# Kernel tuning notes

Hardware: AMD Instinct MI355X
Metric: run time of the kernel (lower is better)

The kernel has to match this reference:

```python
import jax, jax.numpy as jnp
import numpy as np

N = 1024
V = 3889   # SMAL mesh vertices
NJ = 33    # kinematic-tree joints
NR = 35    # rotations in theta (35*3 = 105)
NB = 41    # shape betas
PARENTS = np.concatenate([[0], np.arange(NJ - 1)]).astype(np.int32)  # parent[i] < i
EXTRA_VERT_IDS = np.array([1863, 26, 2124, 150, 3055, 1097])


def _beta_scale_mask():
    m = np.zeros((NR, 3, 6), np.float32)
    leg = list(range(7, 15)) + list(range(17, 25))
    tail = list(range(25, 32))
    ears = [33, 34]
    m[leg, 2, 0] = 1.0; m[leg, 0, 1] = 1.0; m[leg, 1, 1] = 1.0
    m[tail, 0, 2] = 1.0; m[tail, 1, 3] = 1.0; m[tail, 2, 3] = 1.0
    m[ears, 1, 4] = 1.0; m[ears, 2, 5] = 1.0
    return jnp.asarray(m.reshape(NR * 3, 6).T)  # (6, 105)

BETA_SCALE_MASK = _beta_scale_mask()


def batch_rodrigues(theta):
    # theta: (M, 3) axis-angle -> (M, 3, 3) rotation matrices
    angle = jnp.linalg.norm(theta + 1e-8, axis=1, keepdims=True)  # (M,1)
    r = theta / angle
    c = jnp.cos(angle)[..., None]
    s = jnp.sin(angle)[..., None]
    outer = r[:, :, None] * r[:, None, :]
    z = jnp.zeros_like(r[:, 0])
    rx, ry, rz = r[:, 0], r[:, 1], r[:, 2]
    H = jnp.stack([z, -rz, ry, rz, z, -rx, -ry, rx, z], axis=1).reshape(-1, 3, 3)
    eye = jnp.eye(3, dtype=theta.dtype)
    return c * eye + (1.0 - c) * outer + s * H


def make_A(R, t):
    # R: (n,3,3), t: (n,3) -> homogeneous (n,4,4)
    top = jnp.concatenate([R, t[..., None]], axis=-1)
    bottom = jnp.broadcast_to(jnp.array([0.0, 0.0, 0.0, 1.0], dtype=R.dtype), (R.shape[0], 1, 4))
    return jnp.concatenate([top, bottom], axis=1)


def smal_forward(beta, theta, trans, betas_logscale, shapedirs, v_template, J_regressor, posedirs, weights):
    n = beta.shape[0]
    v_shaped = v_template + (beta @ shapedirs).reshape(n, V, 3)           # (n,V,3)
    J = jnp.einsum('nva,vj->nja', v_shaped, J_regressor)                  # (n,33,3)
    Rs = batch_rodrigues(theta.reshape(-1, 3)).reshape(n, NR, 3, 3)
    # pose blendshape term: original multiplies an all-zero pose_feature by posedirs
    v_posed = v_shaped + (jnp.zeros((1, 288), v_shaped.dtype) @ posedirs).reshape(1, V, 3)
    # per-joint anisotropic log-scales
    scal = jnp.exp(betas_logscale @ BETA_SCALE_MASK).reshape(n, NR, 3)    # (n,35,3)
    # kinematic chain (fixed 33-joint loop with parent dependency)
    results = [make_A(Rs[:, 0], J[:, 0])]
    for i in range(1, NJ):
        p = int(PARENTS[i])
        j_here = J[:, i] - J[:, p]
        # diag(1/s_parent) @ R @ diag(s_i), exact inverse of diagonal scale
        rot_new = Rs[:, i] * scal[:, i][:, None, :] / scal[:, p][:, :, None]
        results.append(results[p] @ make_A(rot_new, j_here))
    results = jnp.stack(results, axis=1)                                   # (n,33,4,4)
    init_bone = jnp.einsum('njxk,njk->njx', results[..., :3], J)           # (n,33,4)
    A = jnp.concatenate([results[..., :3], (results[..., 3] - init_bone)[..., None]], axis=-1)
    # linear blend skinning
    T = jnp.einsum('vj,njk->nvk', weights, A.reshape(n, NJ, 16)).reshape(n, V, 4, 4)
    v_homo = jnp.concatenate([v_posed * jnp.ones((n, 1, 1), v_posed.dtype),
                              jnp.ones((n, V, 1), v_posed.dtype)], axis=-1)
    verts = jnp.einsum('nvab,nvb->nva', T, v_homo)[..., :3] + trans[:, None, :]
    joints = jnp.einsum('nva,vj->nja', verts, J_regressor)                 # (n,33,3)
    joints = jnp.concatenate([joints, verts[:, EXTRA_VERT_IDS]], axis=1)   # (n,39,3)
    return verts, joints


def setup_inputs() -> dict:
    key = jax.random.key(0)
    ks = jax.random.split(key, 9)
    return {
        'beta': jax.random.normal(ks[0], (N, NB), jnp.float32) * 0.1,
        'theta': jax.random.normal(ks[1], (N, NR * 3), jnp.float32) * 0.2,
        'trans': jax.random.normal(ks[2], (N, 3), jnp.float32),
        'betas_logscale': jax.random.normal(ks[3], (N, 6), jnp.float32) * 0.1,
        'shapedirs': jax.random.normal(ks[4], (NB, V * 3), jnp.float32) * 0.01,
        'v_template': jax.random.normal(ks[5], (V, 3), jnp.float32),
        'J_regressor': jax.random.uniform(ks[6], (V, NJ), jnp.float32) / V,
        'posedirs': jax.random.normal(ks[7], (288, V * 3), jnp.float32) * 0.01,
        'weights': jax.random.uniform(ks[8], (V, NJ), jnp.float32),
    }


def reference(beta, theta, trans, betas_logscale, shapedirs, v_template, J_regressor, posedirs, weights):
    return smal_forward(beta, theta, trans, betas_logscale, shapedirs, v_template, J_regressor, posedirs, weights)
```

## Files before the change

### kernel.cpp

```cpp
#include <hip/hip_runtime.h>
#include <hip/hip_bf16.h>

#define NV 3889
#define NV3 11667
#define NVP 3904
#define NVAP 11712
#define NJC 33
#define NBB 41
#define NN 1024

__device__ const int EXTRA_IDS[6] = {1863, 26, 2124, 150, 3055, 1097};

#define WS_SJ    0
#define WS_WPK   4160
#define WS_SDPK  129088
#define WS_BPK   503872
#define WS_APK   536640
#define WS_JTL   929856
#define WS_VTL   1028160
#define WS_SJP   13611072

typedef __attribute__((ext_vector_type(8))) short short8v;
typedef __attribute__((ext_vector_type(4))) float f32x4;

__device__ __forceinline__ ushort bf16bits(float x) {
  __hip_bfloat16 h = __float2bfloat16(x);
  return *reinterpret_cast<ushort*>(&h);
}

#define PREP_PACK_BLOCKS 9536
__global__ void __launch_bounds__(256) k_prep(
    const float* __restrict__ Jreg, const float* __restrict__ w,
    const float* __restrict__ beta, const float* __restrict__ sd,
    const float* __restrict__ vt, float* __restrict__ ws) {
  if (blockIdx.x < PREP_PACK_BLOCKS) {
    int id = blockIdx.x * 256 + threadIdx.x;
    const int S1 = NVP * 64;
    const int S2 = NVAP * 64;
    const int S3 = NN * 64;
    const int S4 = 3 * 128 * 512;
    const int S5 = 192 * 6144;
    if (id < S1) {
      int v = id >> 6, j = id & 63;
      float val;
      if (j < NJC)      val = (v < NV) ? w[v * NJC + j] : 0.f;
      else if (j == 41) val = 1.f;
      else              val = 0.f;
      ((__hip_bfloat16*)(ws + WS_WPK))[id] = __float2bfloat16(val);
      return;
    }
    id -= S1;
    if (id < S2) {
      int va = id >> 6, bs = id & 63;
      float val = 0.f;
      if (va < NV3) {
        if (bs < NBB)       val = sd[(size_t)bs * NV3 + va];
        else if (bs == NBB) val = vt[va];
      }
      ((__hip_bfloat16*)(ws + WS_SDPK))[id] = __float2bfloat16(val);
      return;
    }
    id -= S2;
    if (id < S3) {
      int n = id >> 6, bs = id & 63;
      float val = (bs < NBB) ? beta[n * NBB + bs] : (bs == NBB ? 1.f : 0.f);
      ((__hip_bfloat16*)(ws + WS_BPK))[id] = __float2bfloat16(val);
      return;
    }
    id -= S3;
    if (id < S4) {
      int tile = id >> 9, sub = id & 511;
      int lane = sub >> 3, e = sub & 7;
      int jt = tile >> 7, kc = tile & 127;
      int j = jt * 16 + (lane & 15);
      int v = kc * 32 + ((lane >> 4) << 3) + e;
      float val = (j < NJC && v < NV) ? Jreg[v * NJC + j] : 0.f;
      ((__hip_bfloat16*)(ws + WS_JTL))[id] = __float2bfloat16(val);
      return;
    }
    id -= S4;
    if (id < S5) {
      int plane = id / 6144, rem = id - plane * 6144;
      ((ushort*)(ws + WS_VTL))[(size_t)plane * 131072 + 122 * 1024 + rem] = 0;
    }
    return;
  }
  int bid2 = blockIdx.x - PREP_PACK_BLOCKS;
  int b = bid2 >> 4, c = bid2 & 15;
  const float* src = (b < NBB) ? (sd + (size_t)b * NV3) : vt;
  int t = threadIdx.x;
  int dv = t / 33, j = t - dv * 33;
  float p0 = 0.f, p1 = 0.f, p2 = 0.f;
  int vbase = c * 244;
  int vend = vbase + 244;
  if (vend > NV) vend = NV;
  if (t < 231) {
    for (int v0 = vbase; v0 < vend; v0 += 7) {
      int v = v0 + dv;
      if (v < vend) {
        float jr = Jreg[v0 * 33 + t];
        p0 += src[v * 3 + 0] * jr;
        p1 += src[v * 3 + 1] * jr;
        p2 += src[v * 3 + 2] * jr;
      }
    }
  }
  __shared__ float sred[7][33][3];
  if (t < 231) { sred[dv][j][0] = p0; sred[dv][j][1] = p1; sred[dv][j][2] = p2; }
  __syncthreads();
  if (t < 99) {
    int jj = t / 3, aa = t - jj * 3;
    float s = 0.f;
#pragma unroll
    for (int d = 0; d < 7; d++) s += sred[d][jj][aa];
    ws[WS_SJP + bid2 * 100 + t] = s;
  }
}

__global__ void __launch_bounds__(256) k_sjr(float* __restrict__ ws) {
  int idx = blockIdx.x * 256 + threadIdx.x;
  if (idx >= 42 * 99) return;
  int b = idx / 99, k = idx - b * 99;
  float s = 0.f;
#pragma unroll
  for (int c = 0; c < 16; c++) s += ws[WS_SJP + (b * 16 + c) * 100 + k];
  ws[WS_SJ + idx] = s;
}

__device__ __forceinline__ void get_scal(int r, float e0, float e1, float e2, float e3,
                                         float s[3]) {
  bool leg  = (r >= 7 && r <= 14) || (r >= 17 && r <= 24);
  bool tail = (r >= 25 && r <= 31);
  s[0] = leg ? e1 : (tail ? e2 : 1.f);
  s[1] = leg ? e1 : (tail ? e3 : 1.f);
  s[2] = leg ? e0 : (tail ? e3 : 1.f);
}

__device__ __forceinline__ void rodrigues(const float* th, float R[9]) {
  float tx = th[0], ty = th[1], tz = th[2];
  float ax = tx + 1e-8f, ay = ty + 1e-8f, az = tz + 1e-8f;
  float angle = sqrtf(ax * ax + ay * ay + az * az);
  float inv = 1.f / angle;
  float rx = tx * inv, ry = ty * inv, rz = tz * inv;
  float c = cosf(angle), s = sinf(angle), o = 1.f - c;
  R[0] = c + o * rx * rx;      R[1] = o * rx * ry - s * rz; R[2] = o * rx * rz + s * ry;
  R[3] = o * rx * ry + s * rz; R[4] = c + o * ry * ry;      R[5] = o * ry * rz - s * rx;
  R[6] = o * rx * rz - s * ry; R[7] = o * ry * rz + s * rx; R[8] = c + o * rz * rz;
}

__global__ void __launch_bounds__(128) k_pose(
    const float* __restrict__ beta, const float* __restrict__ theta,
    const float* __restrict__ bls, const float* __restrict__ trans,
    float* __restrict__ ws) {
  int n = blockIdx.x, t = threadIdx.x;
  __shared__ float Jsh[99];
  __shared__ float Bsh[NJC * 12];
  __shared__ float Ash[NJC * 12];
  if (t < 99) {
    const float* SJ = ws + WS_SJ;
    float acc = SJ[NBB * 99 + t];
    const float* bn = beta + n * NBB;
#pragma unroll
    for (int b = 0; b < NBB; b++) acc += bn[b] * SJ[b * 99 + t];
    Jsh[t] = acc;
  }
  __syncthreads();
  if (t < NJC) {
    float R[9];
    rodrigues(theta + n * 105 + t * 3, R);
    float* B = Bsh + t * 12;
    if (t == 0) {
      B[0] = R[0]; B[1] = R[1]; B[2]  = R[2]; B[3]  = Jsh[0];
      B[4] = R[3]; B[5] = R[4]; B[6]  = R[5]; B[7]  = Jsh[1];
      B[8] = R[6]; B[9] = R[7]; B[10] = R[8]; B[11] = Jsh[2];
    } else {
      float e0 = expf(bls[n * 6 + 0]), e1 = expf(bls[n * 6 + 1]);
      float e2 = expf(bls[n * 6 + 2]), e3 = expf(bls[n * 6 + 3]);
      float si[3], sp[3];
      get_scal(t, e0, e1, e2, e3, si);
      get_scal(t - 1, e0, e1, e2, e3, sp);
#pragma unroll
      for (int r = 0; r < 3; r++) {
        float inv = 1.f / sp[r];
#pragma unroll
        for (int cc = 0; cc < 3; cc++) B[r * 4 + cc] = R[r * 3 + cc] * si[cc] * inv;
        B[r * 4 + 3] = Jsh[t * 3 + r] - Jsh[(t - 1) * 3 + r];
      }
    }
  }
  __syncthreads();
  if (t == 0) {
    float G[12];
#pragma unroll
    for (int k = 0; k < 12; k++) G[k] = Bsh[k];
#pragma unroll
    for (int i = 0; i < NJC; i++) {
      if (i > 0) {
        float b[12];
#pragma unroll
        for (int k = 0; k < 12; k++) b[k] = Bsh[i * 12 + k];
        float Gn[12];
#pragma unroll
        for (int r = 0; r < 3; r++) {
#pragma unroll
          for (int cc = 0; cc < 4; cc++) {
            float acc = G[r * 4 + 0] * b[0 * 4 + cc] + G[r * 4 + 1] * b[1 * 4 + cc] +
                        G[r * 4 + 2] * b[2 * 4 + cc];
            if (cc == 3) acc += G[r * 4 + 3];
            Gn[r * 4 + cc] = acc;
          }
        }
#pragma unroll
        for (int k = 0; k < 12; k++) G[k] = Gn[k];
      }
      float jx = Jsh[i * 3 + 0], jy = Jsh[i * 3 + 1], jz = Jsh[i * 3 + 2];
      float* Ai = Ash + i * 12;
      Ai[0] = G[0]; Ai[1] = G[1]; Ai[2]  = G[2];
      Ai[3] = G[3] - (G[0] * jx + G[1] * jy + G[2] * jz);
      Ai[4] = G[4]; Ai[5] = G[5]; Ai[6]  = G[6];
      Ai[7] = G[7] - (G[4] * jx + G[5] * jy + G[6] * jz);
      Ai[8] = G[8]; Ai[9] = G[9]; Ai[10] = G[10];
      Ai[11] = G[11] - (G[8] * jx + G[9] * jy + G[10] * jz);
    }
  }
  __syncthreads();
  __hip_bfloat16* apk = (__hip_bfloat16*)(ws + WS_APK) + (size_t)n * 768;
  for (int i = t; i < 768; i += 128) {
    int c = i >> 6, j = i & 63;
    float val = 0.f;
    if (j < NJC)                           val = Ash[j * 12 + c];
    else if (j == 41 && (c & 3) == 3)      val = trans[n * 3 + (c >> 2)];
    apk[i] = __float2bfloat16(val);
  }
}

#define ASH_USH (16 * 12 * 72)
#define VSL2_USH (2 * 16 * 72)

__global__ void __launch_bounds__(512, 4) k_sv(
    const float* __restrict__ ws, ushort* __restrict__ vst,
    float* __restrict__ out) {
  __shared__ __align__(16) ushort lds[ASH_USH + 8 * VSL2_USH];
  int wv = threadIdx.x >> 6, lane = threadIdx.x & 63;
  int g = lane >> 4, c16 = lane & 15;
  int p = blockIdx.x * 8 + wv;
  int pc = p < 122 ? p : 121;
  bool pok = p < 122;
  int vtA = pc * 2, vtB = vtA + 1;
  int vA = vtA * 16 + c16, vB = vtB * 16 + c16;
  int nb0 = blockIdx.y * 32;
  const ushort* Wp = (const ushort*)(ws + WS_WPK);
  const ushort* Sp = (const ushort*)(ws + WS_SDPK);
  const ushort* Bp = (const ushort*)(ws + WS_BPK);
  const ushort* Ap = (const ushort*)(ws + WS_APK);

  short8v wfA0 = *(const short8v*)(Wp + vA * 64 + g * 8);
  short8v wfA1 = *(const short8v*)(Wp + vA * 64 + 32 + g * 8);
  short8v wfB0 = *(const short8v*)(Wp + vB * 64 + g * 8);
  short8v wfB1 = *(const short8v*)(Wp + vB * 64 + 32 + g * 8);
  int vaA = vtA * 48 + c16, vaB = vtB * 48 + c16;

  ushort* vslA = lds + ASH_USH + wv * VSL2_USH;
  ushort* vslB = vslA + 1152;
  bool act = g < 3;
  int hiA = c16 >> 3, hiB = 2 + (c16 >> 3), e8 = c16 & 7;

#pragma unroll 1
  for (int ch = 0; ch < 2; ch++) {
    int nb = nb0 + ch * 16;
    {
      const uint4* srcq = (const uint4*)(Ap + (size_t)nb * 768);
      for (int e = threadIdx.x; e < 1536; e += 512) {
        int r = e >> 3, col = e & 7;
        uint4 x = srcq[e];
        *(uint4*)(lds + r * 72 + col * 8) = x;
      }
    }
    short8v bf0 = *(const short8v*)(Bp + (size_t)(nb + c16) * 64 + g * 8);
    short8v bf1 = *(const short8v*)(Bp + (size_t)(nb + c16) * 64 + 32 + g * 8);
    short8v sfA00 = *(const short8v*)(Sp + (size_t)(vaA +  0) * 64 + g * 8);
    short8v sfA01 = *(const short8v*)(Sp + (size_t)(vaA +  0) * 64 + 32 + g * 8);
    short8v sfA10 = *(const short8v*)(Sp + (size_t)(vaA + 16) * 64 + g * 8);
    short8v sfA11 = *(const short8v*)(Sp + (size_t)(vaA + 16) * 64 + 32 + g * 8);
    short8v sfA20 = *(const short8v*)(Sp + (size_t)(vaA + 32) * 64 + g * 8);
    short8v sfA21 = *(const short8v*)(Sp + (size_t)(vaA + 32) * 64 + 32 + g * 8);
    short8v sfB00 = *(const short8v*)(Sp + (size_t)(vaB +  0) * 64 + g * 8);
    short8v sfB01 = *(const short8v*)(Sp + (size_t)(vaB +  0) * 64 + 32 + g * 8);
    short8v sfB10 = *(const short8v*)(Sp + (size_t)(vaB + 16) * 64 + g * 8);
    short8v sfB11 = *(const short8v*)(Sp + (size_t)(vaB + 16) * 64 + 32 + g * 8);
    short8v sfB20 = *(const short8v*)(Sp + (size_t)(vaB + 32) * 64 + g * 8);
    short8v sfB21 = *(const short8v*)(Sp + (size_t)(vaB + 32) * 64 + 32 + g * 8);
    f32x4 aA0 = {0,0,0,0}, aA1 = {0,0,0,0}, aA2 = {0,0,0,0};
    f32x4 aB0 = {0,0,0,0}, aB1 = {0,0,0,0}, aB2 = {0,0,0,0};
    aA0 = __builtin_amdgcn_mfma_f32_16x16x32_bf16(sfA00, bf0, aA0, 0, 0, 0);
    aA0 = __builtin_amdgcn_mfma_f32_16x16x32_bf16(sfA01, bf1, aA0, 0, 0, 0);
    aA1 = __builtin_amdgcn_mfma_f32_16x16x32_bf16(sfA10, bf0, aA1, 0, 0, 0);
    aA1 = __builtin_amdgcn_mfma_f32_16x16x32_bf16(sfA11, bf1, aA1, 0, 0, 0);
    aA2 = __builtin_amdgcn_mfma_f32_16x16x32_bf16(sfA20, bf0, aA2, 0, 0, 0);
    aA2 = __builtin_amdgcn_mfma_f32_16x16x32_bf16(sfA21, bf1, aA2, 0, 0, 0);
    aB0 = __builtin_amdgcn_mfma_f32_16x16x32_bf16(sfB00, bf0, aB0, 0, 0, 0);
    aB0 = __builtin_amdgcn_mfma_f32_16x16x32_bf16(sfB01, bf1, aB0, 0, 0, 0);
    aB1 = __builtin_amdgcn_mfma_f32_16x16x32_bf16(sfB10, bf0, aB1, 0, 0, 0);
    aB1 = __builtin_amdgcn_mfma_f32_16x16x32_bf16(sfB11, bf1, aB1, 0, 0, 0);
    aB2 = __builtin_amdgcn_mfma_f32_16x16x32_bf16(sfB20, bf0, aB2, 0, 0, 0);
    aB2 = __builtin_amdgcn_mfma_f32_16x16x32_bf16(sfB21, bf1, aB2, 0, 0, 0);
    {
      int wb = c16 * 72;
#pragma unroll
      for (int r = 0; r < 4; r++) {
        int rho = g * 4 + r;
        vslA[wb + (rho / 3) * 4 + (rho % 3)] = bf16bits(aA0[r]);
        vslB[wb + (rho / 3) * 4 + (rho % 3)] = bf16bits(aB0[r]);
      }
#pragma unroll
      for (int r = 0; r < 4; r++) {
        int rho = 16 + g * 4 + r;
        vslA[wb + (rho / 3) * 4 + (rho % 3)] = bf16bits(aA1[r]);
        vslB[wb + (rho / 3) * 4 + (rho % 3)] = bf16bits(aB1[r]);
      }
#pragma unroll
      for (int r = 0; r < 4; r++) {
        int rho = 32 + g * 4 + r;
        vslA[wb + (rho / 3) * 4 + (rho % 3)] = bf16bits(aA2[r]);
        vslB[wb + (rho / 3) * 4 + (rho % 3)] = bf16bits(aB2[r]);
      }
    }
    __syncthreads();

    int nt_w = nb >> 4;
    size_t tbg = ((size_t)((act ? g : 0) * 64 + nt_w) * 128 + pc) * 1024;
#pragma unroll 4
    for (int np = 0; np < 16; np++) {
      const ushort* an = lds + np * 864 + c16 * 72 + g * 8;
      short8v af0 = *(const short8v*)(an);
      short8v af1 = *(const short8v*)(an + 32);
      f32x4 accA = {0,0,0,0}, accB = {0,0,0,0};
      accA = __builtin_amdgcn_mfma_f32_16x16x32_bf16(af0, wfA0, accA, 0, 0, 0);
      accA = __builtin_amdgcn_mfma_f32_16x16x32_bf16(af1, wfA1, accA, 0, 0, 0);
      accB = __builtin_amdgcn_mfma_f32_16x16x32_bf16(af0, wfB0, accB, 0, 0, 0);
      accB = __builtin_amdgcn_mfma_f32_16x16x32_bf16(af1, wfB1, accB, 0, 0, 0);
      uint2 qA = *(const uint2*)(vslA + np * 72 + c16 * 4);
      uint2 qB = *(const uint2*)(vslB + np * 72 + c16 * 4);
      float sxA = __uint_as_float((qA.x & 0xffffu) << 16);
      float syA = __uint_as_float(qA.x & 0xffff0000u);
      float szA = __uint_as_float((qA.y & 0xffffu) << 16);
      float sxB = __uint_as_float((qB.x & 0xffffu) << 16);
      float syB = __uint_as_float(qB.x & 0xffff0000u);
      float szB = __uint_as_float((qB.y & 0xffffu) << 16);
      float rA = fmaf(accA[0], sxA, fmaf(accA[1], syA, fmaf(accA[2], szA, accA[3])));
      float rB = fmaf(accB[0], sxB, fmaf(accB[1], syB, fmaf(accB[2], szB, accB[3])));
      if (pok && act) {
        vst[tbg + (size_t)((hiA * 16 + np) * 8 + e8)] = bf16bits(rA);
        vst[tbg + (size_t)((hiB * 16 + np) * 8 + e8)] = bf16bits(rB);
        out[((size_t)(nb + np) * NV + vA) * 3 + g] = rA;
        if (vB < NV) out[((size_t)(nb + np) * NV + vB) * 3 + g] = rB;
      }
    }
    __syncthreads();
  }
}

__global__ void __launch_bounds__(256) k_jg2(
    const float* __restrict__ ws, const float* __restrict__ verts,
    float* __restrict__ jout) {
  __shared__ float red[4][48][16];
  int nt = blockIdx.x, a = blockIdx.y;
  int wv = threadIdx.x >> 6, lane = threadIdx.x & 63;
  const ushort* Jt = (const ushort*)(ws + WS_JTL);
  const ushort* Vt = (const ushort*)(ws + WS_VTL) + ((size_t)(a * 64 + nt) << 17);
  f32x4 acc0 = {0,0,0,0};
  f32x4 acc1 = {0,0,0,0};
  f32x4 acc2 = {0,0,0,0};
#pragma unroll 4
  for (int i = 0; i < 32; i++) {
    int kc = wv * 32 + i;
    short8v bfr = *(const short8v*)(Vt + ((size_t)kc << 10) + lane * 8);
    short8v af0 = *(const short8v*)(Jt + ((size_t)(0 * 128 + kc) << 9) + lane * 8);
    short8v af1 = *(const short8v*)(Jt + ((size_t)(1 * 128 + kc) << 9) + lane * 8);
    short8v af2 = *(const short8v*)(Jt + ((size_t)(2 * 128 + kc) << 9) + lane * 8);
    acc0 = __builtin_amdgcn_mfma_f32_16x16x32_bf16(af0, bfr, acc0, 0, 0, 0);
    acc1 = __builtin_amdgcn_mfma_f32_16x16x32_bf16(af1, bfr, acc1, 0, 0, 0);
    acc2 = __builtin_amdgcn_mfma_f32_16x16x32_bf16(af2, bfr, acc2, 0, 0, 0);
  }
  int hi = lane >> 4, c16 = lane & 15;
#pragma unroll
  for (int r = 0; r < 4; r++) {
    red[wv][ 0 + hi * 4 + r][c16] = acc0[r];
    red[wv][16 + hi * 4 + r][c16] = acc1[r];
    red[wv][32 + hi * 4 + r][c16] = acc2[r];
  }
  __syncthreads();
  for (int idx = threadIdx.x; idx < NJC * 16; idx += 256) {
    int j = idx >> 4, np = idx & 15;
    float s = red[0][j][np] + red[1][j][np] + red[2][j][np] + red[3][j][np];
    jout[(nt * 16 + np) * 117 + j * 3 + a] = s;
  }
  if (threadIdx.x < 96) {
    int e = threadIdx.x >> 4, np = threadIdx.x & 15;
    int n = nt * 16 + np;
    jout[n * 117 + 99 + e * 3 + a] = verts[(size_t)n * NV3 + EXTRA_IDS[e] * 3 + a];
  }
}

extern "C" void kernel_launch(void* const* d_in, const int* in_sizes, int n_in,
                              void* d_out, int out_size, void* d_ws, size_t ws_size,
                              hipStream_t stream) {
  const float* beta       = (const float*)d_in[0];
  const float* theta      = (const float*)d_in[1];
  const float* trans      = (const float*)d_in[2];
  const float* bls        = (const float*)d_in[3];
  const float* shapedirs  = (const float*)d_in[4];
  const float* v_template = (const float*)d_in[5];
  const float* Jreg       = (const float*)d_in[6];
  const float* weights    = (const float*)d_in[8];
  float* out = (float*)d_out;
  float* ws  = (float*)d_ws;
  float* jout = out + (size_t)NN * NV3;

  k_prep<<<PREP_PACK_BLOCKS + 672, 256, 0, stream>>>(Jreg, weights, beta,
                                                     shapedirs, v_template, ws);
  k_sjr<<<17, 256, 0, stream>>>(ws);
  k_pose<<<NN, 128, 0, stream>>>(beta, theta, bls, trans, ws);
  dim3 gsv(16, 32);
  k_sv<<<gsv, 512, 0, stream>>>(ws, (ushort*)(ws + WS_VTL), out);
  dim3 gj(64, 3);
  k_jg2<<<gj, 256, 0, stream>>>(ws, out, jout);
}
```

Before: 75.91 us.

## Fuse joint regression into skinning kernel and drop bf16 vertex staging buffer

```diff
diff --git a/kernel.cpp b/kernel.cpp
--- a/kernel.cpp
+++ b/kernel.cpp
@@ -17,8 +17,7 @@
 #define WS_BPK   503872
 #define WS_APK   536640
 #define WS_JTL   929856
-#define WS_VTL   1028160
-#define WS_SJP   13611072
+#define WS_JPART 1028160
 
 typedef __attribute__((ext_vector_type(8))) short short8v;
 typedef __attribute__((ext_vector_type(4))) float f32x4;
@@ -28,76 +27,88 @@
   return *reinterpret_cast<ushort*>(&h);
 }
 
-#define PREP_PACK_BLOCKS 9536
+#define PREP_PACK_BLOCKS 616
 __global__ void __launch_bounds__(256) k_prep(
     const float* __restrict__ Jreg, const float* __restrict__ w,
     const float* __restrict__ beta, const float* __restrict__ sd,
     const float* __restrict__ vt, float* __restrict__ ws) {
   if (blockIdx.x < PREP_PACK_BLOCKS) {
-    int id = blockIdx.x * 256 + threadIdx.x;
-    const int S1 = NVP * 64;
-    const int S2 = NVAP * 64;
-    const int S3 = NN * 64;
-    const int S4 = 3 * 128 * 512;
-    const int S5 = 192 * 6144;
-    if (id < S1) {
-      int v = id >> 6, j = id & 63;
-      float val;
-      if (j < NJC)      val = (v < NV) ? w[v * NJC + j] : 0.f;
-      else if (j == 41) val = 1.f;
-      else              val = 0.f;
-      ((__hip_bfloat16*)(ws + WS_WPK))[id] = __float2bfloat16(val);
+    int id8 = blockIdx.x * 256 + threadIdx.x;
+    const int R1 = NVP * 64 / 8;
+    const int R2 = NVAP * 64 / 8;
+    const int R3 = NN * 64 / 8;
+    short8v pk;
+    if (id8 < R1) {
+      int u = id8 * 8;
+      int v = u >> 6, j0 = u & 63;
+#pragma unroll
+      for (int e = 0; e < 8; e++) {
+        int j = j0 + e;
+        float val;
+        if (j < NJC)      val = (v < NV) ? w[v * NJC + j] : 0.f;
+        else if (j == 41) val = 1.f;
+        else              val = 0.f;
+        pk[e] = (short)bf16bits(val);
+      }
+      *(short8v*)((ushort*)(ws + WS_WPK) + u) = pk;
       return;
     }
-    id -= S1;
-    if (id < S2) {
-      int va = id >> 6, bs = id & 63;
-      float val = 0.f;
-      if (va < NV3) {
-        if (bs < NBB)       val = sd[(size_t)bs * NV3 + va];
-        else if (bs == NBB) val = vt[va];
-      }
-      ((__hip_bfloat16*)(ws + WS_SDPK))[id] = __float2bfloat16(val);
+    id8 -= R1;
+    if (id8 < R2) {
+      int u = id8 * 8;
+      int va = u >> 6, bs0 = u & 63;
+#pragma unroll
+      for (int e = 0; e < 8; e++) {
+        int bs = bs0 + e;
+        float val = 0.f;
+        if (va < NV3) {
+          if (bs < NBB)       val = sd[(size_t)bs * NV3 + va];
+          else if (bs == NBB) val = vt[va];
+        }
+        pk[e] = (short)bf16bits(val);
+      }
+      *(short8v*)((ushort*)(ws + WS_SDPK) + u) = pk;
       return;
     }
-    id -= S2;
-    if (id < S3) {
-      int n = id >> 6, bs = id & 63;
-      float val = (bs < NBB) ? beta[n * NBB + bs] : (bs == NBB ? 1.f : 0.f);
-      ((__hip_bfloat16*)(ws + WS_BPK))[id] = __float2bfloat16(val);
+    id8 -= R2;
+    if (id8 < R3) {
+      int u = id8 * 8;
+      int n = u >> 6, bs0 = u & 63;
+#pragma unroll
+      for (int e = 0; e < 8; e++) {
+        int bs = bs0 + e;
+        float val = (bs < NBB) ? beta[n * NBB + bs] : (bs == NBB ? 1.f : 0.f);
+        pk[e] = (short)bf16bits(val);
+      }
+      *(short8v*)((ushort*)(ws + WS_BPK) + u) = pk;
       return;
     }
-    id -= S3;
-    if (id < S4) {
-      int tile = id >> 9, sub = id & 511;
-      int lane = sub >> 3, e = sub & 7;
+    id8 -= R3;
+    {
+      int u = id8 * 8;
+      int tile = u >> 9, lane = (u >> 3) & 63;
       int jt = tile >> 7, kc = tile & 127;
       int j = jt * 16 + (lane & 15);
-      int v = kc * 32 + ((lane >> 4) << 3) + e;
-      float val = (j < NJC && v < NV) ? Jreg[v * NJC + j] : 0.f;
-      ((__hip_bfloat16*)(ws + WS_JTL))[id] = __float2bfloat16(val);
+      int vb = kc * 32 + ((lane >> 4) << 3);
+#pragma unroll
+      for (int e = 0; e < 8; e++) {
+        int v = vb + e;
+        float val = (j < NJC && v < NV) ? Jreg[v * NJC + j] : 0.f;
+        pk[e] = (short)bf16bits(val);
+      }
+      *(short8v*)((ushort*)(ws + WS_JTL) + u) = pk;
       return;
     }
-    id -= S4;
-    if (id < S5) {
-      int plane = id / 6144, rem = id - plane * 6144;
-      ((ushort*)(ws + WS_VTL))[(size_t)plane * 131072 + 122 * 1024 + rem] = 0;
-    }
-    return;
-  }
-  int bid2 = blockIdx.x - PREP_PACK_BLOCKS;
-  int b = bid2 >> 4, c = bid2 & 15;
+  }
+  int b = blockIdx.x - PREP_PACK_BLOCKS;
   const float* src = (b < NBB) ? (sd + (size_t)b * NV3) : vt;
   int t = threadIdx.x;
   int dv = t / 33, j = t - dv * 33;
   float p0 = 0.f, p1 = 0.f, p2 = 0.f;
-  int vbase = c * 244;
-  int vend = vbase + 244;
-  if (vend > NV) vend = NV;
   if (t < 231) {
-    for (int v0 = vbase; v0 < vend; v0 += 7) {
+    for (int v0 = 0; v0 < NV; v0 += 7) {
       int v = v0 + dv;
-      if (v < vend) {
+      if (v < NV) {
         float jr = Jreg[v0 * 33 + t];
         p0 += src[v * 3 + 0] * jr;
         p1 += src[v * 3 + 1] * jr;
@@ -113,18 +124,8 @@
     float s = 0.f;
 #pragma unroll
     for (int d = 0; d < 7; d++) s += sred[d][jj][aa];
-    ws[WS_SJP + bid2 * 100 + t] = s;
-  }
-}
-
-__global__ void __launch_bounds__(256) k_sjr(float* __restrict__ ws) {
-  int idx = blockIdx.x * 256 + threadIdx.x;
-  if (idx >= 42 * 99) return;
-  int b = idx / 99, k = idx - b * 99;
-  float s = 0.f;
-#pragma unroll
-  for (int c = 0; c < 16; c++) s += ws[WS_SJP + (b * 16 + c) * 100 + k];
-  ws[WS_SJ + idx] = s;
+    ws[WS_SJ + b * 99 + t] = s;
+  }
 }
 
 __device__ __forceinline__ void get_scal(int r, float e0, float e1, float e2, float e3,
@@ -235,171 +236,191 @@
 }
 
 #define ASH_USH (16 * 12 * 72)
-#define VSL2_USH (2 * 16 * 72)
-
-__global__ void __launch_bounds__(512, 4) k_sv(
-    const float* __restrict__ ws, ushort* __restrict__ vst,
-    float* __restrict__ out) {
-  __shared__ __align__(16) ushort lds[ASH_USH + 8 * VSL2_USH];
+#define VSL_USH (2 * 16 * 72)
+
+__global__ void __launch_bounds__(512, 4) k_sv2(
+    const float* __restrict__ ws, float* __restrict__ jpart,
+    float* __restrict__ out, float* __restrict__ jout) {
+  __shared__ __align__(16) ushort lds[ASH_USH + 8 * VSL_USH];
   int wv = threadIdx.x >> 6, lane = threadIdx.x & 63;
   int g = lane >> 4, c16 = lane & 15;
-  int p = blockIdx.x * 8 + wv;
-  int pc = p < 122 ? p : 121;
-  bool pok = p < 122;
-  int vtA = pc * 2, vtB = vtA + 1;
-  int vA = vtA * 16 + c16, vB = vtB * 16 + c16;
-  int nb0 = blockIdx.y * 32;
+  int pg = blockIdx.x;
+  int nc = blockIdx.y;
+  int nb = nc * 16;
   const ushort* Wp = (const ushort*)(ws + WS_WPK);
   const ushort* Sp = (const ushort*)(ws + WS_SDPK);
   const ushort* Bp = (const ushort*)(ws + WS_BPK);
   const ushort* Ap = (const ushort*)(ws + WS_APK);
-
-  short8v wfA0 = *(const short8v*)(Wp + vA * 64 + g * 8);
-  short8v wfA1 = *(const short8v*)(Wp + vA * 64 + 32 + g * 8);
-  short8v wfB0 = *(const short8v*)(Wp + vB * 64 + g * 8);
-  short8v wfB1 = *(const short8v*)(Wp + vB * 64 + 32 + g * 8);
-  int vaA = vtA * 48 + c16, vaB = vtB * 48 + c16;
-
-  ushort* vslA = lds + ASH_USH + wv * VSL2_USH;
+  const ushort* Jt = (const ushort*)(ws + WS_JTL);
+
+  {
+    const uint4* srcq = (const uint4*)(Ap + (size_t)nb * 768);
+    for (int e = threadIdx.x; e < 1536; e += 512) {
+      uint4 x = srcq[e];
+      *(uint4*)(lds + (e >> 3) * 72 + (e & 7) * 8) = x;
+    }
+  }
+  __syncthreads();
+
+  short8v bf0 = *(const short8v*)(Bp + (size_t)(nb + c16) * 64 + g * 8);
+  short8v bf1 = *(const short8v*)(Bp + (size_t)(nb + c16) * 64 + 32 + g * 8);
+
+  ushort* vslA = lds + ASH_USH + wv * VSL_USH;
   ushort* vslB = vslA + 1152;
   bool act = g < 3;
-  int hiA = c16 >> 3, hiB = 2 + (c16 >> 3), e8 = c16 & 7;
+
+  f32x4 jc00 = {0,0,0,0}, jc10 = {0,0,0,0}, jc20 = {0,0,0,0};
+  f32x4 jc01 = {0,0,0,0}, jc11 = {0,0,0,0}, jc21 = {0,0,0,0};
+  f32x4 jc02 = {0,0,0,0}, jc12 = {0,0,0,0}, jc22 = {0,0,0,0};
 
 #pragma unroll 1
-  for (int ch = 0; ch < 2; ch++) {
-    int nb = nb0 + ch * 16;
-    {
-      const uint4* srcq = (const uint4*)(Ap + (size_t)nb * 768);
-      for (int e = threadIdx.x; e < 1536; e += 512) {
-        int r = e >> 3, col = e & 7;
-        uint4 x = srcq[e];
-        *(uint4*)(lds + r * 72 + col * 8) = x;
-      }
-    }
-    short8v bf0 = *(const short8v*)(Bp + (size_t)(nb + c16) * 64 + g * 8);
-    short8v bf1 = *(const short8v*)(Bp + (size_t)(nb + c16) * 64 + 32 + g * 8);
-    short8v sfA00 = *(const short8v*)(Sp + (size_t)(vaA +  0) * 64 + g * 8);
-    short8v sfA01 = *(const short8v*)(Sp + (size_t)(vaA +  0) * 64 + 32 + g * 8);
-    short8v sfA10 = *(const short8v*)(Sp + (size_t)(vaA + 16) * 64 + g * 8);
-    short8v sfA11 = *(const short8v*)(Sp + (size_t)(vaA + 16) * 64 + 32 + g * 8);
-    short8v sfA20 = *(const short8v*)(Sp + (size_t)(vaA + 32) * 64 + g * 8);
-    short8v sfA21 = *(const short8v*)(Sp + (size_t)(vaA + 32) * 64 + 32 + g * 8);
-    short8v sfB00 = *(const short8v*)(Sp + (size_t)(vaB +  0) * 64 + g * 8);
-    short8v sfB01 = *(const short8v*)(Sp + (size_t)(vaB +  0) * 64 + 32 + g * 8);
-    short8v sfB10 = *(const short8v*)(Sp + (size_t)(vaB + 16) * 64 + g * 8);
-    short8v sfB11 = *(const short8v*)(Sp + (size_t)(vaB + 16) * 64 + 32 + g * 8);
-    short8v sfB20 = *(const short8v*)(Sp + (size_t)(vaB + 32) * 64 + g * 8);
-    short8v sfB21 = *(const short8v*)(Sp + (size_t)(vaB + 32) * 64 + 32 + g * 8);
-    f32x4 aA0 = {0,0,0,0}, aA1 = {0,0,0,0}, aA2 = {0,0,0,0};
-    f32x4 aB0 = {0,0,0,0}, aB1 = {0,0,0,0}, aB2 = {0,0,0,0};
-    aA0 = __builtin_amdgcn_mfma_f32_16x16x32_bf16(sfA00, bf0, aA0, 0, 0, 0);
-    aA0 = __builtin_amdgcn_mfma_f32_16x16x32_bf16(sfA01, bf1, aA0, 0, 0, 0);
-    aA1 = __builtin_amdgcn_mfma_f32_16x16x32_bf16(sfA10, bf0, aA1, 0, 0, 0);
-    aA1 = __builtin_amdgcn_mfma_f32_16x16x32_bf16(sfA11, bf1, aA1, 0, 0, 0);
-    aA2 = __builtin_amdgcn_mfma_f32_16x16x32_bf16(sfA20, bf0, aA2, 0, 0, 0);
-    aA2 = __builtin_amdgcn_mfma_f32_16x16x32_bf16(sfA21, bf1, aA2, 0, 0, 0);
-    aB0 = __builtin_amdgcn_mfma_f32_16x16x32_bf16(sfB00, bf0, aB0, 0, 0, 0);
-    aB0 = __builtin_amdgcn_mfma_f32_16x16x32_bf16(sfB01, bf1, aB0, 0, 0, 0);
-    aB1 = __builtin_amdgcn_mfma_f32_16x16x32_bf16(sfB10, bf0, aB1, 0, 0, 0);
-    aB1 = __builtin_amdgcn_mfma_f32_16x16x32_bf16(sfB11, bf1, aB1, 0, 0, 0);
-    aB2 = __builtin_amdgcn_mfma_f32_16x16x32_bf16(sfB20, bf0, aB2, 0, 0, 0);
-    aB2 = __builtin_amdgcn_mfma_f32_16x16x32_bf16(sfB21, bf1, aB2, 0, 0, 0);
-    {
-      int wb = c16 * 72;
-#pragma unroll
-      for (int r = 0; r < 4; r++) {
-        int rho = g * 4 + r;
-        vslA[wb + (rho / 3) * 4 + (rho % 3)] = bf16bits(aA0[r]);
-        vslB[wb + (rho / 3) * 4 + (rho % 3)] = bf16bits(aB0[r]);
-      }
-#pragma unroll
-      for (int r = 0; r < 4; r++) {
-        int rho = 16 + g * 4 + r;
-        vslA[wb + (rho / 3) * 4 + (rho % 3)] = bf16bits(aA1[r]);
-        vslB[wb + (rho / 3) * 4 + (rho % 3)] = bf16bits(aB1[r]);
-      }
-#pragma unroll
-      for (int r = 0; r < 4; r++) {
-        int rho = 32 + g * 4 + r;
-        vslA[wb + (rho / 3) * 4 + (rho % 3)] = bf16bits(aA2[r]);
-        vslB[wb + (rho / 3) * 4 + (rho % 3)] = bf16bits(aB2[r]);
-      }
-    }
-    __syncthreads();
-
-    int nt_w = nb >> 4;
-    size_t tbg = ((size_t)((act ? g : 0) * 64 + nt_w) * 128 + pc) * 1024;
+  for (int r = 0; r < 2; r++) {
+    int p = pg * 16 + r * 8 + wv;
+    if (p < 122) {
+      int vtA = p * 2, vtB = vtA + 1;
+      int vA = vtA * 16 + c16, vB = vtB * 16 + c16;
+      int vaA = vtA * 48 + c16, vaB = vtB * 48 + c16;
+      {
+        short8v s00 = *(const short8v*)(Sp + (size_t)(vaA +  0) * 64 + g * 8);
+        short8v s01 = *(const short8v*)(Sp + (size_t)(vaA +  0) * 64 + 32 + g * 8);
+        short8v s10 = *(const short8v*)(Sp + (size_t)(vaA + 16) * 64 + g * 8);
+        short8v s11 = *(const short8v*)(Sp + (size_t)(vaA + 16) * 64 + 32 + g * 8);
+        short8v s20 = *(const short8v*)(Sp + (size_t)(vaA + 32) * 64 + g * 8);
+        short8v s21 = *(const short8v*)(Sp + (size_t)(vaA + 32) * 64 + 32 + g * 8);
+        f32x4 a0 = {0,0,0,0}, a1 = {0,0,0,0}, a2 = {0,0,0,0};
+        a0 = __builtin_amdgcn_mfma_f32_16x16x32_bf16(s00, bf0, a0, 0, 0, 0);
+        a0 = __builtin_amdgcn_mfma_f32_16x16x32_bf16(s01, bf1, a0, 0, 0, 0);
+        a1 = __builtin_amdgcn_mfma_f32_16x16x32_bf16(s10, bf0, a1, 0, 0, 0);
+        a1 = __builtin_amdgcn_mfma_f32_16x16x32_bf16(s11, bf1, a1, 0, 0, 0);
+        a2 = __builtin_amdgcn_mfma_f32_16x16x32_bf16(s20, bf0, a2, 0, 0, 0);
+        a2 = __builtin_amdgcn_mfma_f32_16x16x32_bf16(s21, bf1, a2, 0, 0, 0);
+        int wb = c16 * 72;
+#pragma unroll
+        for (int rr = 0; rr < 4; rr++) {
+          int rho = g * 4 + rr;
+          vslA[wb + (rho / 3) * 4 + (rho % 3)] = bf16bits(a0[rr]);
+          rho = 16 + g * 4 + rr;
+          vslA[wb + (rho / 3) * 4 + (rho % 3)] = bf16bits(a1[rr]);
+          rho = 32 + g * 4 + rr;
+          vslA[wb + (rho / 3) * 4 + (rho % 3)] = bf16bits(a2[rr]);
+        }
+      }
+      {
+        short8v s00 = *(const short8v*)(Sp + (size_t)(vaB +  0) * 64 + g * 8);
+        short8v s01 = *(const short8v*)(Sp + (size_t)(vaB +  0) * 64 + 32 + g * 8);
+        short8v s10 = *(const short8v*)(Sp + (size_t)(vaB + 16) * 64 + g * 8);
+        short8v s11 = *(const short8v*)(Sp + (size_t)(vaB + 16) * 64 + 32 + g * 8);
+        short8v s20 = *(const short8v*)(Sp + (size_t)(vaB + 32) * 64 + g * 8);
+        short8v s21 = *(const short8v*)(Sp + (size_t)(vaB + 32) * 64 + 32 + g * 8);
+        f32x4 a0 = {0,0,0,0}, a1 = {0,0,0,0}, a2 = {0,0,0,0};
+        a0 = __builtin_amdgcn_mfma_f32_16x16x32_bf16(s00, bf0, a0, 0, 0, 0);
+        a0 = __builtin_amdgcn_mfma_f32_16x16x32_bf16(s01, bf1, a0, 0, 0, 0);
+        a1 = __builtin_amdgcn_mfma_f32_16x16x32_bf16(s10, bf0, a1, 0, 0, 0);
+        a1 = __builtin_amdgcn_mfma_f32_16x16x32_bf16(s11, bf1, a1, 0, 0, 0);
+        a2 = __builtin_amdgcn_mfma_f32_16x16x32_bf16(s20, bf0, a2, 0, 0, 0);
+        a2 = __builtin_amdgcn_mfma_f32_16x16x32_bf16(s21, bf1, a2, 0, 0, 0);
+        int wb = c16 * 72;
+#pragma unroll
+        for (int rr = 0; rr < 4; rr++) {
+          int rho = g * 4 + rr;
+          vslB[wb + (rho / 3) * 4 + (rho % 3)] = bf16bits(a0[rr]);
+          rho = 16 + g * 4 + rr;
+          vslB[wb + (rho / 3) * 4 + (rho % 3)] = bf16bits(a1[rr]);
+          rho = 32 + g * 4 + rr;
+          vslB[wb + (rho / 3) * 4 + (rho % 3)] = bf16bits(a2[rr]);
+        }
+      }
+      short8v wfA0 = *(const short8v*)(Wp + (size_t)vA * 64 + g * 8);
+      short8v wfA1 = *(const short8v*)(Wp + (size_t)vA * 64 + 32 + g * 8);
+      short8v wfB0 = *(const short8v*)(Wp + (size_t)vB * 64 + g * 8);
+      short8v wfB1 = *(const short8v*)(Wp + (size_t)vB * 64 + 32 + g * 8);
+      int exA = -1, exB = -1;
+#pragma unroll
+      for (int e = 0; e < 6; e++) {
+        if (vA == EXTRA_IDS[e]) exA = e;
+        if (vB == EXTRA_IDS[e]) exB = e;
+      }
 #pragma unroll 4
-    for (int np = 0; np < 16; np++) {
-      const ushort* an = lds + np * 864 + c16 * 72 + g * 8;
-      short8v af0 = *(const short8v*)(an);
-      short8v af1 = *(const short8v*)(an + 32);
-      f32x4 accA = {0,0,0,0}, accB = {0,0,0,0};
-      accA = __builtin_amdgcn_mfma_f32_16x16x32_bf16(af0, wfA0, accA, 0, 0, 0);
-      accA = __builtin_amdgcn_mfma_f32_16x16x32_bf16(af1, wfA1, accA, 0, 0, 0);
-      accB = __builtin_amdgcn_mfma_f32_16x16x32_bf16(af0, wfB0, accB, 0, 0, 0);
-      accB = __builtin_amdgcn_mfma_f32_16x16x32_bf16(af1, wfB1, accB, 0, 0, 0);
-      uint2 qA = *(const uint2*)(vslA + np * 72 + c16 * 4);
-      uint2 qB = *(const uint2*)(vslB + np * 72 + c16 * 4);
-      float sxA = __uint_as_float((qA.x & 0xffffu) << 16);
-      float syA = __uint_as_float(qA.x & 0xffff0000u);
-      float szA = __uint_as_float((qA.y & 0xffffu) << 16);
-      float sxB = __uint_as_float((qB.x & 0xffffu) << 16);
-      float syB = __uint_as_float(qB.x & 0xffff0000u);
-      float szB = __uint_as_float((qB.y & 0xffffu) << 16);
-      float rA = fmaf(accA[0], sxA, fmaf(accA[1], syA, fmaf(accA[2], szA, accA[3])));
-      float rB = fmaf(accB[0], sxB, fmaf(accB[1], syB, fmaf(accB[2], szB, accB[3])));
-      if (pok && act) {
-        vst[tbg + (size_t)((hiA * 16 + np) * 8 + e8)] = bf16bits(rA);
-        vst[tbg + (size_t)((hiB * 16 + np) * 8 + e8)] = bf16bits(rB);
-        out[((size_t)(nb + np) * NV + vA) * 3 + g] = rA;
-        if (vB < NV) out[((size_t)(nb + np) * NV + vB) * 3 + g] = rB;
-      }
-    }
-    __syncthreads();
-  }
-}
-
-__global__ void __launch_bounds__(256) k_jg2(
-    const float* __restrict__ ws, const float* __restrict__ verts,
-    float* __restrict__ jout) {
-  __shared__ float red[4][48][16];
-  int nt = blockIdx.x, a = blockIdx.y;
-  int wv = threadIdx.x >> 6, lane = threadIdx.x & 63;
-  const ushort* Jt = (const ushort*)(ws + WS_JTL);
-  const ushort* Vt = (const ushort*)(ws + WS_VTL) + ((size_t)(a * 64 + nt) << 17);
-  f32x4 acc0 = {0,0,0,0};
-  f32x4 acc1 = {0,0,0,0};
-  f32x4 acc2 = {0,0,0,0};
-#pragma unroll 4
-  for (int i = 0; i < 32; i++) {
-    int kc = wv * 32 + i;
-    short8v bfr = *(const short8v*)(Vt + ((size_t)kc << 10) + lane * 8);
-    short8v af0 = *(const short8v*)(Jt + ((size_t)(0 * 128 + kc) << 9) + lane * 8);
-    short8v af1 = *(const short8v*)(Jt + ((size_t)(1 * 128 + kc) << 9) + lane * 8);
-    short8v af2 = *(const short8v*)(Jt + ((size_t)(2 * 128 + kc) << 9) + lane * 8);
-    acc0 = __builtin_amdgcn_mfma_f32_16x16x32_bf16(af0, bfr, acc0, 0, 0, 0);
-    acc1 = __builtin_amdgcn_mfma_f32_16x16x32_bf16(af1, bfr, acc1, 0, 0, 0);
-    acc2 = __builtin_amdgcn_mfma_f32_16x16x32_bf16(af2, bfr, acc2, 0, 0, 0);
-  }
-  int hi = lane >> 4, c16 = lane & 15;
-#pragma unroll
-  for (int r = 0; r < 4; r++) {
-    red[wv][ 0 + hi * 4 + r][c16] = acc0[r];
-    red[wv][16 + hi * 4 + r][c16] = acc1[r];
-    red[wv][32 + hi * 4 + r][c16] = acc2[r];
-  }
-  __syncthreads();
-  for (int idx = threadIdx.x; idx < NJC * 16; idx += 256) {
-    int j = idx >> 4, np = idx & 15;
-    float s = red[0][j][np] + red[1][j][np] + red[2][j][np] + red[3][j][np];
-    jout[(nt * 16 + np) * 117 + j * 3 + a] = s;
-  }
-  if (threadIdx.x < 96) {
-    int e = threadIdx.x >> 4, np = threadIdx.x & 15;
-    int n = nt * 16 + np;
-    jout[n * 117 + 99 + e * 3 + a] = verts[(size_t)n * NV3 + EXTRA_IDS[e] * 3 + a];
-  }
+      for (int np = 0; np < 16; np++) {
+        const ushort* an = lds + np * 864 + c16 * 72 + g * 8;
+        short8v af0 = *(const short8v*)(an);
+        short8v af1 = *(const short8v*)(an + 32);
+        f32x4 accA = {0,0,0,0}, accB = {0,0,0,0};
+        accA = __builtin_amdgcn_mfma_f32_16x16x32_bf16(af0, wfA0, accA, 0, 0, 0);
+        accA = __builtin_amdgcn_mfma_f32_16x16x32_bf16(af1, wfA1, accA, 0, 0, 0);
+        accB = __builtin_amdgcn_mfma_f32_16x16x32_bf16(af0, wfB0, accB, 0, 0, 0);
+        accB = __builtin_amdgcn_mfma_f32_16x16x32_bf16(af1, wfB1, accB, 0, 0, 0);
+        uint2 qA = *(const uint2*)(vslA + np * 72 + c16 * 4);
+        uint2 qB = *(const uint2*)(vslB + np * 72 + c16 * 4);
+        float sxA = __uint_as_float((qA.x & 0xffffu) << 16);
+        float syA = __uint_as_float(qA.x & 0xffff0000u);
+        float szA = __uint_as_float((qA.y & 0xffffu) << 16);
+        float sxB = __uint_as_float((qB.x & 0xffffu) << 16);
+        float syB = __uint_as_float(qB.x & 0xffff0000u);
+        float szB = __uint_as_float((qB.y & 0xffffu) << 16);
+        float rA = fmaf(accA[0], sxA, fmaf(accA[1], syA, fmaf(accA[2], szA, accA[3])));
+        float rB = fmaf(accB[0], sxB, fmaf(accB[1], syB, fmaf(accB[2], szB, accB[3])));
+        if (act) {
+          out[((size_t)(nb + np) * NV + vA) * 3 + g] = rA;
+          if (vB < NV) out[((size_t)(nb + np) * NV + vB) * 3 + g] = rB;
+          if (exA >= 0) jout[(size_t)(nb + np) * 117 + 99 + exA * 3 + g] = rA;
+          if (exB >= 0) jout[(size_t)(nb + np) * 117 + 99 + exB * 3 + g] = rB;
+          ushort* dst = (g < 2) ? (vslA + np * 72 + g * 32) : (vslB + np * 72);
+          dst[c16]      = bf16bits(rA);
+          dst[16 + c16] = bf16bits(rB);
+        }
+      }
+      short8v ja0 = *(const short8v*)(Jt + ((size_t)(      p) << 9) + lane * 8);
+      short8v ja1 = *(const short8v*)(Jt + ((size_t)(128 + p) << 9) + lane * 8);
+      short8v ja2 = *(const short8v*)(Jt + ((size_t)(256 + p) << 9) + lane * 8);
+      short8v vb0 = *(const short8v*)(vslA + c16 * 72 + g * 8);
+      short8v vb1 = *(const short8v*)(vslA + c16 * 72 + 32 + g * 8);
+      short8v vb2 = *(const short8v*)(vslB + c16 * 72 + g * 8);
+      jc00 = __builtin_amdgcn_mfma_f32_16x16x32_bf16(ja0, vb0, jc00, 0, 0, 0);
+      jc10 = __builtin_amdgcn_mfma_f32_16x16x32_bf16(ja1, vb0, jc10, 0, 0, 0);
+      jc20 = __builtin_amdgcn_mfma_f32_16x16x32_bf16(ja2, vb0, jc20, 0, 0, 0);
+      jc01 = __builtin_amdgcn_mfma_f32_16x16x32_bf16(ja0, vb1, jc01, 0, 0, 0);
+      jc11 = __builtin_amdgcn_mfma_f32_16x16x32_bf16(ja1, vb1, jc11, 0, 0, 0);
+      jc21 = __builtin_amdgcn_mfma_f32_16x16x32_bf16(ja2, vb1, jc21, 0, 0, 0);
+      jc02 = __builtin_amdgcn_mfma_f32_16x16x32_bf16(ja0, vb2, jc02, 0, 0, 0);
+      jc12 = __builtin_amdgcn_mfma_f32_16x16x32_bf16(ja1, vb2, jc12, 0, 0, 0);
+      jc22 = __builtin_amdgcn_mfma_f32_16x16x32_bf16(ja2, vb2, jc22, 0, 0, 0);
+    }
+  }
+
+  __syncthreads();
+  float* sc = (float*)lds;
+  for (int i = threadIdx.x; i < 2304; i += 512) sc[i] = 0.f;
+  __syncthreads();
+  int rb = (g * 4) * 16 + c16;
+#define JADD(JC, A, T)                                         \
+  atomicAdd(sc + ((A) * 3 + (T)) * 256 + rb +  0, JC[0]);      \
+  atomicAdd(sc + ((A) * 3 + (T)) * 256 + rb + 16, JC[1]);      \
+  atomicAdd(sc + ((A) * 3 + (T)) * 256 + rb + 32, JC[2]);      \
+  atomicAdd(sc + ((A) * 3 + (T)) * 256 + rb + 48, JC[3]);
+  JADD(jc00, 0, 0) JADD(jc10, 0, 1) JADD(jc20, 0, 2)
+  JADD(jc01, 1, 0) JADD(jc11, 1, 1) JADD(jc21, 1, 2)
+  JADD(jc02, 2, 0) JADD(jc12, 2, 1) JADD(jc22, 2, 2)
+#undef JADD
+  __syncthreads();
+  float* jp = jpart + ((size_t)pg * 64 + nc) * 2304;
+  for (int i = threadIdx.x; i < 2304; i += 512) jp[i] = sc[i];
+}
+
+__global__ void __launch_bounds__(256) k_jred(
+    const float* __restrict__ jpart, float* __restrict__ jout) {
+  int idx = blockIdx.x * 256 + threadIdx.x;
+  if (idx >= NN * 99) return;
+  int n = idx / 99, k = idx - n * 99;
+  int j = k / 3, a = k - j * 3;
+  int ncb = n >> 4, nl = n & 15;
+  int jt = j >> 4, jl = j & 15;
+  int ofs = ((a * 3 + jt) * 16 + jl) * 16 + nl;
+  const float* base = jpart + (size_t)ncb * 2304 + ofs;
+  float s = 0.f;
+#pragma unroll
+  for (int pgi = 0; pgi < 8; pgi++) s += base[(size_t)pgi * 64 * 2304];
+  jout[(size_t)n * 117 + j * 3 + a] = s;
 }
 
 extern "C" void kernel_launch(void* const* d_in, const int* in_sizes, int n_in,
@@ -416,13 +437,12 @@
   float* out = (float*)d_out;
   float* ws  = (float*)d_ws;
   float* jout = out + (size_t)NN * NV3;
-
-  k_prep<<<PREP_PACK_BLOCKS + 672, 256, 0, stream>>>(Jreg, weights, beta,
-                                                     shapedirs, v_template, ws);
-  k_sjr<<<17, 256, 0, stream>>>(ws);
+  float* jpart = ws + WS_JPART;
+
+  k_prep<<<PREP_PACK_BLOCKS + 42, 256, 0, stream>>>(Jreg, weights, beta,
+                                                    shapedirs, v_template, ws);
   k_pose<<<NN, 128, 0, stream>>>(beta, theta, bls, trans, ws);
-  dim3 gsv(16, 32);
-  k_sv<<<gsv, 512, 0, stream>>>(ws, (ushort*)(ws + WS_VTL), out);
-  dim3 gj(64, 3);
-  k_jg2<<<gj, 256, 0, stream>>>(ws, out, jout);
-}
+  dim3 gsv(8, 64);
+  k_sv2<<<gsv, 512, 0, stream>>>(ws, jpart, out, jout);
+  k_jred<<<(NN * 99 + 255) / 256, 256, 0, stream>>>(jpart, jout);
+}
```

After: 239.1 us. 215% more time.
